# Performance work log

Measured on AMD Instinct MI355X. Metric: run time of the kernel, lower is better.

## Reference

```python
import jax, jax.numpy as jnp
import numpy as np

N_NODES = 20000
N_EDGES = 160000
EPS = 1e-5
LEAKY_SLOPE = 0.01


def gcn_conv(x, src, dst, W, b, num_nodes):
    """PyG GCNConv: self-loops + symmetric normalization. out = D^-1/2 A_hat D^-1/2 (x W) + b."""
    h = x @ W  # [N, out]
    loop = jnp.arange(num_nodes, dtype=src.dtype)
    s = jnp.concatenate([src, loop])
    d = jnp.concatenate([dst, loop])
    deg = jax.ops.segment_sum(jnp.ones_like(d, dtype=h.dtype), d, num_segments=num_nodes)
    dinv = jnp.where(deg > 0, jax.lax.rsqrt(jnp.maximum(deg, 1.0)) * jnp.where(deg > 0, 1.0, 0.0), 0.0)
    norm = dinv[s] * dinv[d]  # [E+N]
    msgs = h[s] * norm[:, None]  # gather + scale (memory-bound)
    out = jax.ops.segment_sum(msgs, d, num_segments=num_nodes)
    return out + b


def setup_inputs() -> dict:
    key = jax.random.key(0)
    ks = jax.random.split(key, 8)
    x = jax.random.normal(ks[0], (N_NODES, 1), dtype=jnp.float32)
    edge_index = jax.random.randint(ks[1], (2, N_EDGES), 0, N_NODES, dtype=jnp.int32)
    s = 0.02
    W1 = jax.random.normal(ks[2], (1, 2048), dtype=jnp.float32) * s
    b1 = jnp.zeros((2048,), jnp.float32)
    W2 = jax.random.normal(ks[3], (2048, 1024), dtype=jnp.float32) * s
    b2 = jnp.zeros((1024,), jnp.float32)
    gamma = jnp.ones((1024,), jnp.float32)
    beta = jnp.zeros((1024,), jnp.float32)
    running_mean = jnp.zeros((1024,), jnp.float32)
    running_var = jnp.ones((1024,), jnp.float32)
    lW1 = jax.random.normal(ks[4], (1024, 256), dtype=jnp.float32) * s
    lb1 = jnp.zeros((256,), jnp.float32)
    lW2 = jax.random.normal(ks[5], (256, 124), dtype=jnp.float32) * s
    lb2 = jnp.zeros((124,), jnp.float32)
    return dict(x=x, edge_index=edge_index, W1=W1, b1=b1, W2=W2, b2=b2,
                gamma=gamma, beta=beta, running_mean=running_mean,
                running_var=running_var, lW1=lW1, lb1=lb1, lW2=lW2, lb2=lb2)


def reference(x, edge_index, W1, b1, W2, b2, gamma, beta,
              running_mean, running_var, lW1, lb1, lW2, lb2):
    n = x.shape[0]
    src, dst = edge_index[0], edge_index[1]
    h = gcn_conv(x, src, dst, W1, b1, n)          # GCNConv(1, 2048); dropout is identity in eval
    h = gcn_conv(h, src, dst, W2, b2, n)          # GCNConv(2048, 1024)
    h = (h - running_mean) * (gamma * jax.lax.rsqrt(running_var + EPS)) + beta  # BatchNorm (eval)
    h = h @ lW1 + lb1                              # Linear 1024->256
    h = jnp.where(h >= 0, h, LEAKY_SLOPE * h)      # LeakyReLU
    h = h @ lW2 + lb2                              # Linear 256->124
    return jax.nn.log_softmax(h, axis=1)
```

## Files before the change

kernel.cpp:

```cpp
#include <hip/hip_runtime.h>
#include <math.h>

#define N_NODES 20000
#define N_EDGES 160000
#define EPSB 1e-5f
#define SLOPE 0.01f

typedef __attribute__((ext_vector_type(8))) short short8;
typedef __attribute__((ext_vector_type(4))) float f32x4;

#define OFF_DEG    0
#define OFF_ACC2   20000
#define OFF_B      60000
#define OFF_V      80000
#define OFF_U      81024
#define OFF_R      82048
#define OFF_RU     82304
#define OFF_S      82560
#define OFF_ZEND   82816
#define OFF_Q1     82816
#define OFF_Q2     122816
#define OFF_BFRAG  142816

#define T_STRIDE 264

__device__ __forceinline__ unsigned short f2bf(float f) {
    unsigned u = __float_as_uint(f);
    return (unsigned short)((u + 0x7FFFu + ((u >> 16) & 1u)) >> 16);
}

__global__ void K1_deg_v_bf(const int* __restrict__ dst, int* __restrict__ deg,
                            const float* __restrict__ W1, const float* __restrict__ b1,
                            const float* __restrict__ W2, const float* __restrict__ lW2,
                            float* __restrict__ v, float* __restrict__ u,
                            unsigned short* __restrict__ bfrag) {
    int b = blockIdx.x;
    if (b < 625) {
        int e = b * 256 + threadIdx.x;
        atomicAdd(&deg[dst[e]], 1);
    } else if (b < 881) {
        int bb = b - 625;
        int k  = (bb & 3) * 256 + threadIdx.x;
        int c0 = (bb >> 2) * 32;
        float av = 0.f, au = 0.f;
        for (int c = c0; c < c0 + 32; ++c) {
            float w = W2[c * 1024 + k];
            av = fmaf(W1[c], w, av);
            au = fmaf(b1[c], w, au);
        }
        unsafeAtomicAdd(&v[k], av);
        unsafeAtomicAdd(&u[k], au);
    } else {
        int i = (b - 881) * 256 + threadIdx.x;
        int ct = i >> 9, ks = (i >> 6) & 7, lane = i & 63;
        int n  = ct * 16 + (lane & 15);
        int kb = ks * 32 + (lane >> 4) * 8;
        union { unsigned short u8[8]; short8 v8; } pk;
#pragma unroll
        for (int j = 0; j < 8; ++j)
            pk.u8[j] = (n < 124) ? f2bf(lW2[(kb + j) * 124 + n]) : (unsigned short)0;
        ((short8*)bfrag)[i] = pk.v8;
    }
}

__global__ void K2_q1_rs(const int* __restrict__ deg, const float* __restrict__ x,
                         float2* __restrict__ q1,
                         const float* __restrict__ v, const float* __restrict__ u,
                         const float* __restrict__ gamma, const float* __restrict__ beta,
                         const float* __restrict__ mean, const float* __restrict__ var,
                         const float* __restrict__ b2, const float* __restrict__ lW1,
                         const float* __restrict__ lb1,
                         float* __restrict__ r, float* __restrict__ ru, float* __restrict__ s) {
    int b = blockIdx.x;
    if (b < 79) {
        int n = b * 256 + threadIdx.x;
        if (n < N_NODES) {
            float dinv = rsqrtf((float)(deg[n] + 1));
            float2 q; q.x = dinv * x[n]; q.y = dinv;
            q1[n] = q;
        }
    } else {
        int bb = b - 79, m = threadIdx.x, k0 = bb * 32;
        float ar = 0.f, aru = 0.f, as = 0.f;
        for (int k = k0; k < k0 + 32; ++k) {
            float g = gamma[k] * rsqrtf(var[k] + EPSB);
            float w = lW1[k * 256 + m];
            ar  = fmaf(v[k] * g, w, ar);
            aru = fmaf(u[k] * g, w, aru);
            as  = fmaf(fmaf(b2[k] - mean[k], g, beta[k]), w, as);
        }
        if (bb == 0) as += lb1[m];
        unsafeAtomicAdd(&r[m], ar);
        unsafeAtomicAdd(&ru[m], aru);
        unsafeAtomicAdd(&s[m], as);
    }
}

__global__ void K3_edges1(const int* __restrict__ src, const int* __restrict__ dst,
                          const float2* __restrict__ q1, float* __restrict__ acc2) {
    int e = blockIdx.x * 256 + threadIdx.x;
    int sn = src[e], d = dst[e];
    float2 q = q1[sn];
    unsafeAtomicAdd(&acc2[2 * d],     q.x);
    unsafeAtomicAdd(&acc2[2 * d + 1], q.y);
}

__global__ void K4_q2(const float2* __restrict__ q1, const float2* __restrict__ acc2,
                      float* __restrict__ q2) {
    int n = blockIdx.x * 256 + threadIdx.x;
    if (n < N_NODES) {
        float2 q  = q1[n];
        float2 ac = acc2[n];
        float agg1f = q.y * (ac.x + q.x);
        q2[n] = q.y * agg1f;
    }
}

__global__ void K5_edges2(const int* __restrict__ src, const int* __restrict__ dst,
                          const float* __restrict__ q2, float* __restrict__ B) {
    int e = blockIdx.x * 256 + threadIdx.x;
    unsafeAtomicAdd(&B[dst[e]], q2[src[e]]);
}

__global__ __launch_bounds__(256, 2) void F_final(
    const float2* __restrict__ q1, const float* __restrict__ q2,
    const float* __restrict__ B, const float2* __restrict__ acc2,
    const float* __restrict__ r, const float* __restrict__ ru,
    const float* __restrict__ s,
    const short8* __restrict__ bfrag, const float* __restrict__ lb2,
    float* __restrict__ out) {
    __shared__ unsigned short tsh[16 * T_STRIDE];
    __shared__ float a_sh[16], cn_sh[16];
    __shared__ float logits[16 * 132];
    int tid  = threadIdx.x;
    int lane = tid & 63;
    int wave = __builtin_amdgcn_readfirstlane(tid >> 6);
    int row  = lane & 15, quad = lane >> 4;

    short8 bf0[8], bf1[8];
#pragma unroll
    for (int ks = 0; ks < 8; ++ks) {
        bf0[ks] = bfrag[((wave * 2 + 0) * 8 + ks) * 64 + lane];
        bf1[ks] = bfrag[((wave * 2 + 1) * 8 + ks) * 64 + lane];
    }
    float cr = r[tid], cu = ru[tid], cs = s[tid];

    for (int it = 0; it < 2; ++it) {
        int node0 = (blockIdx.x * 2 + it) * 16;
        if (tid < 16) {
            int n = node0 + tid;
            float2 q = q1[n];
            float dinv = q.y;
            a_sh[tid]  = dinv * (B[n] + q2[n]);
            cn_sh[tid] = dinv * (acc2[n].y + dinv);
        }
        __syncthreads();

#pragma unroll
        for (int n = 0; n < 16; ++n) {
            float t = fmaf(cn_sh[n], cu, fmaf(a_sh[n], cr, cs));
            t = fmaf(SLOPE, fminf(t, 0.f), fmaxf(t, 0.f));
            tsh[n * T_STRIDE + tid] = f2bf(t);
        }
        __syncthreads();

        f32x4 acc0 = {0.f, 0.f, 0.f, 0.f}, acc1 = {0.f, 0.f, 0.f, 0.f};
        const unsigned short* tb = &tsh[row * T_STRIDE + quad * 8];
#pragma unroll
        for (int ks = 0; ks < 8; ++ks) {
            short8 af = *(const short8*)(tb + ks * 32);
            acc0 = __builtin_amdgcn_mfma_f32_16x16x32_bf16(af, bf0[ks], acc0, 0, 0, 0);
            acc1 = __builtin_amdgcn_mfma_f32_16x16x32_bf16(af, bf1[ks], acc1, 0, 0, 0);
        }
        int colbase = wave * 32;
#pragma unroll
        for (int rg = 0; rg < 4; ++rg) {
            int rw = quad * 4 + rg;
            logits[rw * 132 + colbase + row]      = acc0[rg];
            logits[rw * 132 + colbase + 16 + row] = acc1[rg];
        }
        __syncthreads();

        int nd = tid >> 4, sub = tid & 15, c0 = sub * 8;
        int jend = 124 - c0; if (jend > 8) jend = 8;
        float vbuf[8];
        const float* lrow = &logits[nd * 132 + c0];
        float mx = -1e30f;
        for (int j = 0; j < jend; ++j) {
            vbuf[j] = lrow[j] + lb2[c0 + j];
            mx = fmaxf(mx, vbuf[j]);
        }
        mx = fmaxf(mx, __shfl_xor(mx, 1, 16));
        mx = fmaxf(mx, __shfl_xor(mx, 2, 16));
        mx = fmaxf(mx, __shfl_xor(mx, 4, 16));
        mx = fmaxf(mx, __shfl_xor(mx, 8, 16));
        float sm = 0.f;
        for (int j = 0; j < jend; ++j) sm += __expf(vbuf[j] - mx);
        sm += __shfl_xor(sm, 1, 16);
        sm += __shfl_xor(sm, 2, 16);
        sm += __shfl_xor(sm, 4, 16);
        sm += __shfl_xor(sm, 8, 16);
        float lz = mx + __logf(sm);
        float* orow = out + (node0 + nd) * 124 + c0;
        for (int j = 0; j < jend; ++j) orow[j] = vbuf[j] - lz;
    }
}

extern "C" void kernel_launch(void* const* d_in, const int* in_sizes, int n_in,
                              void* d_out, int out_size, void* d_ws, size_t ws_size,
                              hipStream_t stream) {
    const float* x     = (const float*)d_in[0];
    const int*   ei    = (const int*)d_in[1];
    const int*   src   = ei;
    const int*   dst   = ei + N_EDGES;
    const float* W1    = (const float*)d_in[2];
    const float* b1    = (const float*)d_in[3];
    const float* W2    = (const float*)d_in[4];
    const float* b2    = (const float*)d_in[5];
    const float* gamma = (const float*)d_in[6];
    const float* beta  = (const float*)d_in[7];
    const float* rmean = (const float*)d_in[8];
    const float* rvar  = (const float*)d_in[9];
    const float* lW1   = (const float*)d_in[10];
    const float* lb1   = (const float*)d_in[11];
    const float* lW2   = (const float*)d_in[12];
    const float* lb2   = (const float*)d_in[13];
    float* out = (float*)d_out;
    float* ws  = (float*)d_ws;

    int*    deg  = (int*)(ws + OFF_DEG);
    float*  acc2 = ws + OFF_ACC2;
    float*  B    = ws + OFF_B;
    float*  v    = ws + OFF_V;
    float*  u    = ws + OFF_U;
    float*  r    = ws + OFF_R;
    float*  ru   = ws + OFF_RU;
    float*  s    = ws + OFF_S;
    float2* q1   = (float2*)(ws + OFF_Q1);
    float*  q2   = ws + OFF_Q2;
    unsigned short* bfrag = (unsigned short*)(ws + OFF_BFRAG);

    hipMemsetAsync(ws, 0, OFF_ZEND * sizeof(float), stream);

    K1_deg_v_bf<<<625 + 256 + 16, 256, 0, stream>>>(dst, deg, W1, b1, W2, lW2, v, u, bfrag);
    K2_q1_rs<<<79 + 32, 256, 0, stream>>>(deg, x, q1, v, u, gamma, beta,
                                          rmean, rvar, b2, lW1, lb1, r, ru, s);
    K3_edges1<<<625, 256, 0, stream>>>(src, dst, q1, acc2);
    K4_q2<<<79, 256, 0, stream>>>(q1, (const float2*)acc2, q2);
    K5_edges2<<<625, 256, 0, stream>>>(src, dst, q2, B);
    F_final<<<625, 256, 0, stream>>>(q1, q2, B, (const float2*)acc2,
                                     r, ru, s, (const short8*)bfrag, lb2, out);
}
```

Before: 159.3 us.

## Fuse all stages into one cooperative persistent kernel with grid syncs

Replaces the six separate kernel launches with a single cooperative kernel of 512 persistent blocks. Stages are separated by grid.sync() and each stage uses grid-stride loops. The aim is to remove per-launch overhead and inter-kernel gaps, which matter because every stage is tiny. In exchange it pays for five grid-wide barriers, and the final MFMA stage loops over tiles with fewer blocks, so load balance and occupancy may suffer.

```diff
diff --git a/kernel.cpp b/kernel.cpp
--- a/kernel.cpp
+++ b/kernel.cpp
@@ -1,10 +1,15 @@
 #include <hip/hip_runtime.h>
+#include <hip/hip_cooperative_groups.h>
 #include <math.h>
+
+namespace cg = cooperative_groups;
 
 #define N_NODES 20000
 #define N_EDGES 160000
 #define EPSB 1e-5f
 #define SLOPE 0.01f
+#define NB 512
+#define NTHR (NB * 256)
 
 typedef __attribute__((ext_vector_type(8))) short short8;
 typedef __attribute__((ext_vector_type(4))) float f32x4;
@@ -29,110 +34,111 @@
     return (unsigned short)((u + 0x7FFFu + ((u >> 16) & 1u)) >> 16);
 }
 
-__global__ void K1_deg_v_bf(const int* __restrict__ dst, int* __restrict__ deg,
-                            const float* __restrict__ W1, const float* __restrict__ b1,
-                            const float* __restrict__ W2, const float* __restrict__ lW2,
-                            float* __restrict__ v, float* __restrict__ u,
-                            unsigned short* __restrict__ bfrag) {
-    int b = blockIdx.x;
-    if (b < 625) {
-        int e = b * 256 + threadIdx.x;
-        atomicAdd(&deg[dst[e]], 1);
-    } else if (b < 881) {
-        int bb = b - 625;
-        int k  = (bb & 3) * 256 + threadIdx.x;
-        int c0 = (bb >> 2) * 32;
-        float av = 0.f, au = 0.f;
-        for (int c = c0; c < c0 + 32; ++c) {
-            float w = W2[c * 1024 + k];
-            av = fmaf(W1[c], w, av);
-            au = fmaf(b1[c], w, au);
-        }
-        unsafeAtomicAdd(&v[k], av);
-        unsafeAtomicAdd(&u[k], au);
-    } else {
-        int i = (b - 881) * 256 + threadIdx.x;
-        int ct = i >> 9, ks = (i >> 6) & 7, lane = i & 63;
-        int n  = ct * 16 + (lane & 15);
-        int kb = ks * 32 + (lane >> 4) * 8;
-        union { unsigned short u8[8]; short8 v8; } pk;
-#pragma unroll
-        for (int j = 0; j < 8; ++j)
-            pk.u8[j] = (n < 124) ? f2bf(lW2[(kb + j) * 124 + n]) : (unsigned short)0;
-        ((short8*)bfrag)[i] = pk.v8;
-    }
-}
-
-__global__ void K2_q1_rs(const int* __restrict__ deg, const float* __restrict__ x,
-                         float2* __restrict__ q1,
-                         const float* __restrict__ v, const float* __restrict__ u,
-                         const float* __restrict__ gamma, const float* __restrict__ beta,
-                         const float* __restrict__ mean, const float* __restrict__ var,
-                         const float* __restrict__ b2, const float* __restrict__ lW1,
-                         const float* __restrict__ lb1,
-                         float* __restrict__ r, float* __restrict__ ru, float* __restrict__ s) {
-    int b = blockIdx.x;
-    if (b < 79) {
-        int n = b * 256 + threadIdx.x;
-        if (n < N_NODES) {
-            float dinv = rsqrtf((float)(deg[n] + 1));
-            float2 q; q.x = dinv * x[n]; q.y = dinv;
-            q1[n] = q;
-        }
-    } else {
-        int bb = b - 79, m = threadIdx.x, k0 = bb * 32;
-        float ar = 0.f, aru = 0.f, as = 0.f;
-        for (int k = k0; k < k0 + 32; ++k) {
-            float g = gamma[k] * rsqrtf(var[k] + EPSB);
-            float w = lW1[k * 256 + m];
-            ar  = fmaf(v[k] * g, w, ar);
-            aru = fmaf(u[k] * g, w, aru);
-            as  = fmaf(fmaf(b2[k] - mean[k], g, beta[k]), w, as);
-        }
-        if (bb == 0) as += lb1[m];
-        unsafeAtomicAdd(&r[m], ar);
-        unsafeAtomicAdd(&ru[m], aru);
-        unsafeAtomicAdd(&s[m], as);
-    }
-}
-
-__global__ void K3_edges1(const int* __restrict__ src, const int* __restrict__ dst,
-                          const float2* __restrict__ q1, float* __restrict__ acc2) {
-    int e = blockIdx.x * 256 + threadIdx.x;
-    int sn = src[e], d = dst[e];
-    float2 q = q1[sn];
-    unsafeAtomicAdd(&acc2[2 * d],     q.x);
-    unsafeAtomicAdd(&acc2[2 * d + 1], q.y);
-}
-
-__global__ void K4_q2(const float2* __restrict__ q1, const float2* __restrict__ acc2,
-                      float* __restrict__ q2) {
-    int n = blockIdx.x * 256 + threadIdx.x;
-    if (n < N_NODES) {
-        float2 q  = q1[n];
-        float2 ac = acc2[n];
-        float agg1f = q.y * (ac.x + q.x);
-        q2[n] = q.y * agg1f;
-    }
-}
-
-__global__ void K5_edges2(const int* __restrict__ src, const int* __restrict__ dst,
-                          const float* __restrict__ q2, float* __restrict__ B) {
-    int e = blockIdx.x * 256 + threadIdx.x;
-    unsafeAtomicAdd(&B[dst[e]], q2[src[e]]);
-}
-
-__global__ __launch_bounds__(256, 2) void F_final(
-    const float2* __restrict__ q1, const float* __restrict__ q2,
-    const float* __restrict__ B, const float2* __restrict__ acc2,
-    const float* __restrict__ r, const float* __restrict__ ru,
-    const float* __restrict__ s,
-    const short8* __restrict__ bfrag, const float* __restrict__ lb2,
-    float* __restrict__ out) {
+__global__ __launch_bounds__(256, 2) void fused_all(
+    const float* __restrict__ x, const int* __restrict__ src, const int* __restrict__ dst,
+    const float* __restrict__ W1, const float* __restrict__ b1,
+    const float* __restrict__ W2, const float* __restrict__ b2,
+    const float* __restrict__ gamma, const float* __restrict__ beta,
+    const float* __restrict__ mean, const float* __restrict__ var,
+    const float* __restrict__ lW1, const float* __restrict__ lb1,
+    const float* __restrict__ lW2, const float* __restrict__ lb2,
+    float* __restrict__ ws, float* __restrict__ out)
+{
+    cg::grid_group grid = cg::this_grid();
+    int tid = threadIdx.x, bid = blockIdx.x;
+
+    int*    deg  = (int*)(ws + OFF_DEG);
+    float*  acc2 = ws + OFF_ACC2;
+    float*  Bv   = ws + OFF_B;
+    float*  v    = ws + OFF_V;
+    float*  u    = ws + OFF_U;
+    float*  r    = ws + OFF_R;
+    float*  ru   = ws + OFF_RU;
+    float*  s    = ws + OFF_S;
+    float2* q1   = (float2*)(ws + OFF_Q1);
+    float*  q2   = ws + OFF_Q2;
+    unsigned short* bfrag = (unsigned short*)(ws + OFF_BFRAG);
+
     __shared__ unsigned short tsh[16 * T_STRIDE];
     __shared__ float a_sh[16], cn_sh[16];
     __shared__ float logits[16 * 132];
-    int tid  = threadIdx.x;
+
+    for (int ub = bid; ub < 897; ub += NB) {
+        if (ub < 625) {
+            int e = ub * 256 + tid;
+            atomicAdd(&deg[dst[e]], 1);
+        } else if (ub < 881) {
+            int bb = ub - 625;
+            int k  = (bb & 3) * 256 + tid;
+            int c0 = (bb >> 2) * 32;
+            float av = 0.f, au = 0.f;
+            for (int c = c0; c < c0 + 32; ++c) {
+                float w = W2[c * 1024 + k];
+                av = fmaf(W1[c], w, av);
+                au = fmaf(b1[c], w, au);
+            }
+            unsafeAtomicAdd(&v[k], av);
+            unsafeAtomicAdd(&u[k], au);
+        } else {
+            int i = (ub - 881) * 256 + tid;
+            int ct = i >> 9, ks = (i >> 6) & 7, lane = i & 63;
+            int n  = ct * 16 + (lane & 15);
+            int kb = ks * 32 + (lane >> 4) * 8;
+            union { unsigned short u8[8]; short8 v8; } pk;
+#pragma unroll
+            for (int j = 0; j < 8; ++j)
+                pk.u8[j] = (n < 124) ? f2bf(lW2[(kb + j) * 124 + n]) : (unsigned short)0;
+            ((short8*)bfrag)[i] = pk.v8;
+        }
+    }
+    grid.sync();
+
+    for (int ub = bid; ub < 111; ub += NB) {
+        if (ub < 79) {
+            int n = ub * 256 + tid;
+            if (n < N_NODES) {
+                float dinv = rsqrtf((float)(deg[n] + 1));
+                float2 q; q.x = dinv * x[n]; q.y = dinv;
+                q1[n] = q;
+            }
+        } else {
+            int bb = ub - 79, m = tid, k0 = bb * 32;
+            float ar = 0.f, aru = 0.f, as = 0.f;
+            for (int k = k0; k < k0 + 32; ++k) {
+                float g = gamma[k] * rsqrtf(var[k] + EPSB);
+                float w = lW1[k * 256 + m];
+                ar  = fmaf(v[k] * g, w, ar);
+                aru = fmaf(u[k] * g, w, aru);
+                as  = fmaf(fmaf(b2[k] - mean[k], g, beta[k]), w, as);
+            }
+            if (bb == 0) as += lb1[m];
+            unsafeAtomicAdd(&r[m], ar);
+            unsafeAtomicAdd(&ru[m], aru);
+            unsafeAtomicAdd(&s[m], as);
+        }
+    }
+    grid.sync();
+
+    for (int e = bid * 256 + tid; e < N_EDGES; e += NTHR) {
+        int sn = src[e], d = dst[e];
+        float2 q = q1[sn];
+        unsafeAtomicAdd(&acc2[2 * d],     q.x);
+        unsafeAtomicAdd(&acc2[2 * d + 1], q.y);
+    }
+    grid.sync();
+
+    for (int n = bid * 256 + tid; n < N_NODES; n += NTHR) {
+        float2 q  = q1[n];
+        float2 ac = ((const float2*)acc2)[n];
+        q2[n] = q.y * q.y * (ac.x + q.x);
+    }
+    grid.sync();
+
+    for (int e = bid * 256 + tid; e < N_EDGES; e += NTHR) {
+        unsafeAtomicAdd(&Bv[dst[e]], q2[src[e]]);
+    }
+    grid.sync();
+
     int lane = tid & 63;
     int wave = __builtin_amdgcn_readfirstlane(tid >> 6);
     int row  = lane & 15, quad = lane >> 4;
@@ -140,27 +146,27 @@
     short8 bf0[8], bf1[8];
 #pragma unroll
     for (int ks = 0; ks < 8; ++ks) {
-        bf0[ks] = bfrag[((wave * 2 + 0) * 8 + ks) * 64 + lane];
-        bf1[ks] = bfrag[((wave * 2 + 1) * 8 + ks) * 64 + lane];
+        bf0[ks] = ((const short8*)bfrag)[((wave * 2 + 0) * 8 + ks) * 64 + lane];
+        bf1[ks] = ((const short8*)bfrag)[((wave * 2 + 1) * 8 + ks) * 64 + lane];
     }
     float cr = r[tid], cu = ru[tid], cs = s[tid];
 
-    for (int it = 0; it < 2; ++it) {
-        int node0 = (blockIdx.x * 2 + it) * 16;
+    for (int t = bid; t < 1250; t += NB) {
+        int node0 = t * 16;
         if (tid < 16) {
             int n = node0 + tid;
             float2 q = q1[n];
             float dinv = q.y;
-            a_sh[tid]  = dinv * (B[n] + q2[n]);
-            cn_sh[tid] = dinv * (acc2[n].y + dinv);
+            a_sh[tid]  = dinv * (Bv[n] + q2[n]);
+            cn_sh[tid] = dinv * (((const float2*)acc2)[n].y + dinv);
         }
         __syncthreads();
 
 #pragma unroll
         for (int n = 0; n < 16; ++n) {
-            float t = fmaf(cn_sh[n], cu, fmaf(a_sh[n], cr, cs));
-            t = fmaf(SLOPE, fminf(t, 0.f), fmaxf(t, 0.f));
-            tsh[n * T_STRIDE + tid] = f2bf(t);
+            float tt = fmaf(cn_sh[n], cu, fmaf(a_sh[n], cr, cs));
+            tt = fmaf(SLOPE, fminf(tt, 0.f), fmaxf(tt, 0.f));
+            tsh[n * T_STRIDE + tid] = f2bf(tt);
         }
         __syncthreads();
 
@@ -228,26 +234,14 @@
     float* out = (float*)d_out;
     float* ws  = (float*)d_ws;
 
-    int*    deg  = (int*)(ws + OFF_DEG);
-    float*  acc2 = ws + OFF_ACC2;
-    float*  B    = ws + OFF_B;
-    float*  v    = ws + OFF_V;
-    float*  u    = ws + OFF_U;
-    float*  r    = ws + OFF_R;
-    float*  ru   = ws + OFF_RU;
-    float*  s    = ws + OFF_S;
-    float2* q1   = (float2*)(ws + OFF_Q1);
-    float*  q2   = ws + OFF_Q2;
-    unsigned short* bfrag = (unsigned short*)(ws + OFF_BFRAG);
-
     hipMemsetAsync(ws, 0, OFF_ZEND * sizeof(float), stream);
 
-    K1_deg_v_bf<<<625 + 256 + 16, 256, 0, stream>>>(dst, deg, W1, b1, W2, lW2, v, u, bfrag);
-    K2_q1_rs<<<79 + 32, 256, 0, stream>>>(deg, x, q1, v, u, gamma, beta,
-                                          rmean, rvar, b2, lW1, lb1, r, ru, s);
-    K3_edges1<<<625, 256, 0, stream>>>(src, dst, q1, acc2);
-    K4_q2<<<79, 256, 0, stream>>>(q1, (const float2*)acc2, q2);
-    K5_edges2<<<625, 256, 0, stream>>>(src, dst, q2, B);
-    F_final<<<625, 256, 0, stream>>>(q1, q2, B, (const float2*)acc2,
-                                     r, ru, s, (const short8*)bfrag, lb2, out);
+    void* args[] = {
+        (void*)&x, (void*)&src, (void*)&dst,
+        (void*)&W1, (void*)&b1, (void*)&W2, (void*)&b2,
+        (void*)&gamma, (void*)&beta, (void*)&rmean, (void*)&rvar,
+        (void*)&lW1, (void*)&lb1, (void*)&lW2, (void*)&lb2,
+        (void*)&ws, (void*)&out
+    };
+    hipLaunchCooperativeKernel((void*)fused_all, dim3(NB), dim3(256), args, 0, stream);
 }
```

After: 450.9 us. 2.83x slower.

## Fuse edge passes with node setup kernels to cut launch count from six to four

Applied to the files above, without the earlier changes.

The first edge-scatter pass now computes each source node's dinv from the degree array directly, so it can run in the same launch as the q1 computation and the r/ru/s reduction. The q2 node kernel is removed. q2 is recomputed inline in the second edge pass and in the final kernel from q1 and acc2, which also drops the q2 buffer. This saves two kernel launches and their sync points, at the cost of an extra rsqrt and degree gather per edge and an additional acc2 gather in the second edge pass.

```diff
diff --git a/kernel.cpp b/kernel.cpp
--- a/kernel.cpp
+++ b/kernel.cpp
@@ -19,8 +19,7 @@
 #define OFF_S      82560
 #define OFF_ZEND   82816
 #define OFF_Q1     82816
-#define OFF_Q2     122816
-#define OFF_BFRAG  142816
+#define OFF_BFRAG  122816
 
 #define T_STRIDE 264
 
@@ -29,7 +28,7 @@
     return (unsigned short)((u + 0x7FFFu + ((u >> 16) & 1u)) >> 16);
 }
 
-__global__ void K1_deg_v_bf(const int* __restrict__ dst, int* __restrict__ deg,
+__global__ void E1_deg_v_bf(const int* __restrict__ dst, int* __restrict__ deg,
                             const float* __restrict__ W1, const float* __restrict__ b1,
                             const float* __restrict__ W2, const float* __restrict__ lW2,
                             float* __restrict__ v, float* __restrict__ u,
@@ -63,24 +62,25 @@
     }
 }
 
-__global__ void K2_q1_rs(const int* __restrict__ deg, const float* __restrict__ x,
-                         float2* __restrict__ q1,
-                         const float* __restrict__ v, const float* __restrict__ u,
-                         const float* __restrict__ gamma, const float* __restrict__ beta,
-                         const float* __restrict__ mean, const float* __restrict__ var,
-                         const float* __restrict__ b2, const float* __restrict__ lW1,
-                         const float* __restrict__ lb1,
-                         float* __restrict__ r, float* __restrict__ ru, float* __restrict__ s) {
+__global__ void E2_edges1_rs_q1(const int* __restrict__ src, const int* __restrict__ dst,
+                                const int* __restrict__ deg, const float* __restrict__ x,
+                                float* __restrict__ acc2, float2* __restrict__ q1,
+                                const float* __restrict__ v, const float* __restrict__ u,
+                                const float* __restrict__ gamma, const float* __restrict__ beta,
+                                const float* __restrict__ mean, const float* __restrict__ var,
+                                const float* __restrict__ b2, const float* __restrict__ lW1,
+                                const float* __restrict__ lb1,
+                                float* __restrict__ r, float* __restrict__ ru,
+                                float* __restrict__ s) {
     int b = blockIdx.x;
-    if (b < 79) {
-        int n = b * 256 + threadIdx.x;
-        if (n < N_NODES) {
-            float dinv = rsqrtf((float)(deg[n] + 1));
-            float2 q; q.x = dinv * x[n]; q.y = dinv;
-            q1[n] = q;
-        }
-    } else {
-        int bb = b - 79, m = threadIdx.x, k0 = bb * 32;
+    if (b < 625) {
+        int e = b * 256 + threadIdx.x;
+        int sn = src[e], d = dst[e];
+        float dinv = rsqrtf((float)(deg[sn] + 1));
+        unsafeAtomicAdd(&acc2[2 * d],     dinv * x[sn]);
+        unsafeAtomicAdd(&acc2[2 * d + 1], dinv);
+    } else if (b < 657) {
+        int bb = b - 625, m = threadIdx.x, k0 = bb * 32;
         float ar = 0.f, aru = 0.f, as = 0.f;
         for (int k = k0; k < k0 + 32; ++k) {
             float g = gamma[k] * rsqrtf(var[k] + EPSB);
@@ -93,38 +93,29 @@
         unsafeAtomicAdd(&r[m], ar);
         unsafeAtomicAdd(&ru[m], aru);
         unsafeAtomicAdd(&s[m], as);
-    }
-}
-
-__global__ void K3_edges1(const int* __restrict__ src, const int* __restrict__ dst,
-                          const float2* __restrict__ q1, float* __restrict__ acc2) {
+    } else {
+        int n = (b - 657) * 256 + threadIdx.x;
+        if (n < N_NODES) {
+            float dinv = rsqrtf((float)(deg[n] + 1));
+            float2 q; q.x = dinv * x[n]; q.y = dinv;
+            q1[n] = q;
+        }
+    }
+}
+
+__global__ void E3_edges2(const int* __restrict__ src, const int* __restrict__ dst,
+                          const float2* __restrict__ q1, const float2* __restrict__ acc2,
+                          float* __restrict__ B) {
     int e = blockIdx.x * 256 + threadIdx.x;
     int sn = src[e], d = dst[e];
-    float2 q = q1[sn];
-    unsafeAtomicAdd(&acc2[2 * d],     q.x);
-    unsafeAtomicAdd(&acc2[2 * d + 1], q.y);
-}
-
-__global__ void K4_q2(const float2* __restrict__ q1, const float2* __restrict__ acc2,
-                      float* __restrict__ q2) {
-    int n = blockIdx.x * 256 + threadIdx.x;
-    if (n < N_NODES) {
-        float2 q  = q1[n];
-        float2 ac = acc2[n];
-        float agg1f = q.y * (ac.x + q.x);
-        q2[n] = q.y * agg1f;
-    }
-}
-
-__global__ void K5_edges2(const int* __restrict__ src, const int* __restrict__ dst,
-                          const float* __restrict__ q2, float* __restrict__ B) {
-    int e = blockIdx.x * 256 + threadIdx.x;
-    unsafeAtomicAdd(&B[dst[e]], q2[src[e]]);
+    float2 q  = q1[sn];
+    float2 ac = acc2[sn];
+    unsafeAtomicAdd(&B[d], q.y * q.y * (ac.x + q.x));
 }
 
 __global__ __launch_bounds__(256, 2) void F_final(
-    const float2* __restrict__ q1, const float* __restrict__ q2,
-    const float* __restrict__ B, const float2* __restrict__ acc2,
+    const float2* __restrict__ q1, const float2* __restrict__ acc2,
+    const float* __restrict__ B,
     const float* __restrict__ r, const float* __restrict__ ru,
     const float* __restrict__ s,
     const short8* __restrict__ bfrag, const float* __restrict__ lb2,
@@ -149,10 +140,12 @@
         int node0 = (blockIdx.x * 2 + it) * 16;
         if (tid < 16) {
             int n = node0 + tid;
-            float2 q = q1[n];
+            float2 q  = q1[n];
+            float2 ac = acc2[n];
             float dinv = q.y;
-            a_sh[tid]  = dinv * (B[n] + q2[n]);
-            cn_sh[tid] = dinv * (acc2[n].y + dinv);
+            float q2n  = dinv * dinv * (ac.x + q.x);
+            a_sh[tid]  = dinv * (B[n] + q2n);
+            cn_sh[tid] = dinv * (ac.y + dinv);
         }
         __syncthreads();
 
@@ -237,17 +230,15 @@
     float*  ru   = ws + OFF_RU;
     float*  s    = ws + OFF_S;
     float2* q1   = (float2*)(ws + OFF_Q1);
-    float*  q2   = ws + OFF_Q2;
     unsigned short* bfrag = (unsigned short*)(ws + OFF_BFRAG);
 
     hipMemsetAsync(ws, 0, OFF_ZEND * sizeof(float), stream);
 
-    K1_deg_v_bf<<<625 + 256 + 16, 256, 0, stream>>>(dst, deg, W1, b1, W2, lW2, v, u, bfrag);
-    K2_q1_rs<<<79 + 32, 256, 0, stream>>>(deg, x, q1, v, u, gamma, beta,
-                                          rmean, rvar, b2, lW1, lb1, r, ru, s);
-    K3_edges1<<<625, 256, 0, stream>>>(src, dst, q1, acc2);
-    K4_q2<<<79, 256, 0, stream>>>(q1, (const float2*)acc2, q2);
-    K5_edges2<<<625, 256, 0, stream>>>(src, dst, q2, B);
-    F_final<<<625, 256, 0, stream>>>(q1, q2, B, (const float2*)acc2,
-                                     r, ru, s, (const short8*)bfrag, lb2, out);
-}
+    E1_deg_v_bf<<<625 + 256 + 16, 256, 0, stream>>>(dst, deg, W1, b1, W2, lW2, v, u, bfrag);
+    E2_edges1_rs_q1<<<625 + 32 + 79, 256, 0, stream>>>(src, dst, deg, x, acc2, q1,
+                                                       v, u, gamma, beta, rmean, rvar,
+                                                       b2, lW1, lb1, r, ru, s);
+    E3_edges2<<<625, 256, 0, stream>>>(src, dst, q1, (const float2*)acc2, B);
+    F_final<<<625, 256, 0, stream>>>(q1, (const float2*)acc2, B, r, ru, s,
+                                     (const short8*)bfrag, lb2, out);
+}
```

Measured after the change: 151.5 us. 4.9% less time.
